# Kernel tuning notes

Hardware: AMD Instinct MI355X
Metric: run time of the kernel (lower is better)

The kernel has to match this reference:

```python
import jax, jax.numpy as jnp
import numpy as np
import math

N_WIRES = 8
DIM = 2 ** N_WIRES  # 256

# Pauli-Z sign table: wire 0 is the most-significant axis of the statevector.
_idx = np.arange(DIM)
_SIGNS = np.stack([1.0 - 2.0 * ((_idx >> (N_WIRES - 1 - w)) & 1) for w in range(N_WIRES)], axis=1).astype(np.float32)  # [256, 8]


def _cnot(state, c, t):
    # state: [N, 2, 2, ..., 2]; flip target axis where control bit == 1
    s0, s1 = jnp.split(state, 2, axis=1 + c)
    s1 = jnp.flip(s1, axis=1 + t)
    return jnp.concatenate([s0, s1], axis=1 + c)


def _quantum_heads(x, theta):
    """Simulate the QLayer circuit. x: [N, 8] -> PauliZ expectations [N, 8].

    Circuit: RX(x_i) then RX(theta_i) on wire i (commute -> RX(x_i+theta_i)),
    CNOT chain (0,1)...(6,7),(7,0), MeasureAll(PauliZ).
    """
    phi = 0.5 * (x + theta)  # RX half-angle
    c = jnp.cos(phi)
    s = jnp.sin(phi)
    # RX(a)|0> = cos(a/2)|0> - i sin(a/2)|1>
    amps = jax.lax.complex(jnp.stack([c, jnp.zeros_like(c)], axis=-1),
                           jnp.stack([jnp.zeros_like(s), -s], axis=-1))  # [N, 8, 2] complex64
    # Product state as rank-8 tensor [N, 2, ..., 2]
    state = amps[:, 0]
    for w in range(1, N_WIRES):
        state = state[..., None] * amps[:, w].reshape((-1,) + (1,) * w + (2,))
    # Entangling CNOT ring
    for w in range(N_WIRES - 1):
        state = _cnot(state, w, w + 1)
    state = _cnot(state, N_WIRES - 1, 0)
    probs = jnp.abs(state.reshape(-1, DIM)) ** 2  # [N, 256]
    return probs @ jnp.asarray(_SIGNS)  # [N, 8]


def setup_inputs() -> dict:
    key = jax.random.key(0)
    k1, k2, k3, k4 = jax.random.split(key, 4)
    B, S, E = 32, 512, 64
    return {
        "x": jax.random.normal(k1, (B, S, E), dtype=jnp.float32),
        "theta": jax.random.normal(k2, (N_WIRES,), dtype=jnp.float32),
        "W": jax.random.normal(k3, (E, E), dtype=jnp.float32) * 0.05,
        "b": jax.random.normal(k4, (E,), dtype=jnp.float32) * 0.05,
    }


def reference(x, theta, W, b):
    B, S, E = x.shape
    H = E // N_WIRES  # num_heads
    # q = k = v: same deterministic quantum projection applied to the same x.
    z = _quantum_heads(x.reshape(B * S * H, N_WIRES), theta).reshape(B, S, H, N_WIRES)
    scale = 1.0 / math.sqrt(E // H)
    # NOTE: matmul over last dims -> attention across heads within each token.
    scores = jnp.einsum('bshd,bstd->bsht', z, z) * scale  # [B, S, H, H]
    attn = jax.nn.softmax(scores, axis=-1)
    out = jnp.einsum('bsht,bstd->bshd', attn, z).reshape(B, S, E)
    return out @ W.T + b
```

## Files before the change

kernel.cpp:

```cpp
#include <hip/hip_runtime.h>


#define TOK_PER_BLK 16

typedef __attribute__((ext_vector_type(8))) short short8;
typedef __attribute__((ext_vector_type(4))) float f32x4;

__device__ inline unsigned short f2bf(float f) {
    unsigned u = __float_as_uint(f);
    u += 0x7FFF + ((u >> 16) & 1);
    return (unsigned short)(u >> 16);
}

__device__ inline short8 pack_bf16x8(float4 a, float4 b) {
    short8 r;
    r[0] = (short)f2bf(a.x); r[1] = (short)f2bf(a.y);
    r[2] = (short)f2bf(a.z); r[3] = (short)f2bf(a.w);
    r[4] = (short)f2bf(b.x); r[5] = (short)f2bf(b.y);
    r[6] = (short)f2bf(b.z); r[7] = (short)f2bf(b.w);
    return r;
}

__global__ __launch_bounds__(128, 2)
void mhaq_fused4(const float* __restrict__ x,
                 const float* __restrict__ theta,
                 const float* __restrict__ W,
                 const float* __restrict__ bias,
                 float* __restrict__ out,
                 int n_tokens)
{
    __shared__ __align__(16) float          zs[TOK_PER_BLK * 68];
    __shared__ __align__(16) unsigned short os[TOK_PER_BLK * 72];

    const int tid  = threadIdx.x;
    const int lane = tid & 63;
    const int wave = tid >> 6;
    const int lr   = lane & 15;
    const int lg   = lane >> 4;
    const int blockbase = blockIdx.x * TOK_PER_BLK;

    float4 wf[2][2][2];
    float  bj[2];
    {
        const float4* __restrict__ Wv = reinterpret_cast<const float4*>(W);
        #pragma unroll
        for (int nt = 0; nt < 2; ++nt) {
            int j = wave * 32 + nt * 16 + lr;
            bj[nt] = bias[j];
            #pragma unroll
            for (int kt = 0; kt < 2; ++kt) {
                int fidx = (j * 64 + kt * 32 + lg * 8) >> 2;
                wf[nt][kt][0] = Wv[fidx];
                wf[nt][kt][1] = Wv[fidx + 1];
            }
        }
    }

    const int tl = tid >> 3;
    const int g  = tid & 7;
    const int token = blockbase + tl;
    const bool valid = token < n_tokens;
    float zh[8];
    {
        float4 a  = make_float4(0.f, 0.f, 0.f, 0.f);
        float4 b4 = make_float4(0.f, 0.f, 0.f, 0.f);
        if (valid) {
            const float4* __restrict__ xp =
                reinterpret_cast<const float4*>(x) + (size_t)token * 16 + g * 2;
            a = xp[0]; b4 = xp[1];
        }
        float c0 = __cosf(a.x  + theta[0]);
        float c1 = __cosf(a.y  + theta[1]);
        float c2 = __cosf(a.z  + theta[2]);
        float c3 = __cosf(a.w  + theta[3]);
        float c4 = __cosf(b4.x + theta[4]);
        float c5 = __cosf(b4.y + theta[5]);
        float c6 = __cosf(b4.z + theta[6]);
        float c7 = __cosf(b4.w + theta[7]);
        float p1 = c0 * c1;
        float p2 = p1 * c2;
        float p3 = p2 * c3;
        float p4 = p3 * c4;
        float p5 = p4 * c5;
        float p6 = p5 * c6;
        float p7 = p6 * c7;
        float s6 = c6 * c7;
        float s5 = c5 * s6;
        float s4 = c4 * s5;
        float s3 = c3 * s4;
        float s2 = c2 * s3;
        float s1 = c1 * s2;
        zh[0] = s1; zh[1] = p1; zh[2] = p2; zh[3] = p3;
        zh[4] = p4; zh[5] = p5; zh[6] = p6; zh[7] = p7;

        float4* z4 = reinterpret_cast<float4*>(zs + tl * 68 + g * 8);
        z4[0] = make_float4(zh[0], zh[1], zh[2], zh[3]);
        z4[1] = make_float4(zh[4], zh[5], zh[6], zh[7]);
    }
    __syncthreads();

    {
        __align__(16) float zf[64];
        const float* zrow = zs + tl * 68;
        #pragma unroll
        for (int k4 = 0; k4 < 16; ++k4)
            *reinterpret_cast<float4*>(&zf[4 * k4]) =
                *reinterpret_cast<const float4*>(&zrow[4 * k4]);

        const float scale = 0.35355339059327373f;
        float sc[8];
        #pragma unroll
        for (int t = 0; t < 8; ++t) {
            float s = 0.f;
            #pragma unroll
            for (int d = 0; d < 8; ++d)
                s = fmaf(zh[d], zf[t * 8 + d], s);
            sc[t] = __expf(s * scale);
        }
        float sum = sc[0] + sc[1] + sc[2] + sc[3]
                  + sc[4] + sc[5] + sc[6] + sc[7];
        float inv = 1.0f / sum;

        unsigned short oh[8];
        #pragma unroll
        for (int d = 0; d < 8; ++d) {
            float acc = 0.f;
            #pragma unroll
            for (int t = 0; t < 8; ++t)
                acc = fmaf(sc[t], zf[t * 8 + d], acc);
            oh[d] = f2bf(acc * inv);
        }
        ushort4* o4 = reinterpret_cast<ushort4*>(&os[tl * 72 + g * 8]);
        o4[0] = make_ushort4(oh[0], oh[1], oh[2], oh[3]);
        o4[1] = make_ushort4(oh[4], oh[5], oh[6], oh[7]);
    }
    __syncthreads();

    {
        short8 afrag[2];
        #pragma unroll
        for (int kt = 0; kt < 2; ++kt)
            afrag[kt] = *reinterpret_cast<const short8*>(
                &os[lr * 72 + kt * 32 + lg * 8]);

        #pragma unroll
        for (int nt = 0; nt < 2; ++nt) {
            int j = wave * 32 + nt * 16 + lr;
            f32x4 acc = {bj[nt], bj[nt], bj[nt], bj[nt]};
            #pragma unroll
            for (int kt = 0; kt < 2; ++kt) {
                short8 bfrag = pack_bf16x8(wf[nt][kt][0], wf[nt][kt][1]);
                acc = __builtin_amdgcn_mfma_f32_16x16x32_bf16(
                    afrag[kt], bfrag, acc, 0, 0, 0);
            }
            #pragma unroll
            for (int r = 0; r < 4; ++r) {
                int trow = blockbase + lg * 4 + r;
                if (trow < n_tokens)
                    out[(size_t)trow * 64 + j] = acc[r];
            }
        }
    }
}

extern "C" void kernel_launch(void* const* d_in, const int* in_sizes, int n_in,
                              void* d_out, int out_size, void* d_ws, size_t ws_size,
                              hipStream_t stream)
{
    const float* x     = (const float*)d_in[0];
    const float* theta = (const float*)d_in[1];
    const float* W     = (const float*)d_in[2];
    const float* b     = (const float*)d_in[3];
    float* out         = (float*)d_out;

    const int n_tokens = in_sizes[0] / 64;
    const int blocks   = (n_tokens + TOK_PER_BLK - 1) / TOK_PER_BLK;
    mhaq_fused4<<<blocks, 128, 0, stream>>>(x, theta, W, b, out, n_tokens);
}
```

Baseline: 9.858 us.

## Double threads per block, split attention per head across two lanes

```diff
diff --git a/kernel.cpp b/kernel.cpp
--- a/kernel.cpp
+++ b/kernel.cpp
@@ -21,8 +21,8 @@
     return r;
 }
 
-__global__ __launch_bounds__(128, 2)
-void mhaq_fused4(const float* __restrict__ x,
+__global__ __launch_bounds__(256, 4)
+void mhaq_fused5(const float* __restrict__ x,
                  const float* __restrict__ theta,
                  const float* __restrict__ W,
                  const float* __restrict__ bias,
@@ -33,50 +33,48 @@
     __shared__ __align__(16) unsigned short os[TOK_PER_BLK * 72];
 
     const int tid  = threadIdx.x;
+    const int tl   = tid >> 4;
+    const int s    = tid & 15;
+    const int h    = s >> 1;
+    const int half = s & 1;
+    const int blockbase = blockIdx.x * TOK_PER_BLK;
+    const int token = blockbase + tl;
+    const bool zrole = (s < 8);
+
+    float4 xa = make_float4(0.f, 0.f, 0.f, 0.f);
+    float4 xb = make_float4(0.f, 0.f, 0.f, 0.f);
+    if (zrole && token < n_tokens) {
+        const float4* __restrict__ xp =
+            reinterpret_cast<const float4*>(x) + (size_t)token * 16 + s * 2;
+        xa = xp[0]; xb = xp[1];
+    }
+
     const int lane = tid & 63;
     const int wave = tid >> 6;
     const int lr   = lane & 15;
     const int lg   = lane >> 4;
-    const int blockbase = blockIdx.x * TOK_PER_BLK;
-
-    float4 wf[2][2][2];
-    float  bj[2];
+    const int j    = wave * 16 + lr;
+    float4 wf[2][2];
+    float  bj = bias[j];
     {
         const float4* __restrict__ Wv = reinterpret_cast<const float4*>(W);
         #pragma unroll
-        for (int nt = 0; nt < 2; ++nt) {
-            int j = wave * 32 + nt * 16 + lr;
-            bj[nt] = bias[j];
-            #pragma unroll
-            for (int kt = 0; kt < 2; ++kt) {
-                int fidx = (j * 64 + kt * 32 + lg * 8) >> 2;
-                wf[nt][kt][0] = Wv[fidx];
-                wf[nt][kt][1] = Wv[fidx + 1];
-            }
+        for (int kt = 0; kt < 2; ++kt) {
+            int fidx = (j * 64 + kt * 32 + lg * 8) >> 2;
+            wf[kt][0] = Wv[fidx];
+            wf[kt][1] = Wv[fidx + 1];
         }
     }
 
-    const int tl = tid >> 3;
-    const int g  = tid & 7;
-    const int token = blockbase + tl;
-    const bool valid = token < n_tokens;
-    float zh[8];
-    {
-        float4 a  = make_float4(0.f, 0.f, 0.f, 0.f);
-        float4 b4 = make_float4(0.f, 0.f, 0.f, 0.f);
-        if (valid) {
-            const float4* __restrict__ xp =
-                reinterpret_cast<const float4*>(x) + (size_t)token * 16 + g * 2;
-            a = xp[0]; b4 = xp[1];
-        }
-        float c0 = __cosf(a.x  + theta[0]);
-        float c1 = __cosf(a.y  + theta[1]);
-        float c2 = __cosf(a.z  + theta[2]);
-        float c3 = __cosf(a.w  + theta[3]);
-        float c4 = __cosf(b4.x + theta[4]);
-        float c5 = __cosf(b4.y + theta[5]);
-        float c6 = __cosf(b4.z + theta[6]);
-        float c7 = __cosf(b4.w + theta[7]);
+    if (zrole) {
+        float c0 = __cosf(xa.x + theta[0]);
+        float c1 = __cosf(xa.y + theta[1]);
+        float c2 = __cosf(xa.z + theta[2]);
+        float c3 = __cosf(xa.w + theta[3]);
+        float c4 = __cosf(xb.x + theta[4]);
+        float c5 = __cosf(xb.y + theta[5]);
+        float c6 = __cosf(xb.z + theta[6]);
+        float c7 = __cosf(xb.w + theta[7]);
         float p1 = c0 * c1;
         float p2 = p1 * c2;
         float p3 = p2 * c3;
@@ -90,49 +88,70 @@
         float s3 = c3 * s4;
         float s2 = c2 * s3;
         float s1 = c1 * s2;
-        zh[0] = s1; zh[1] = p1; zh[2] = p2; zh[3] = p3;
-        zh[4] = p4; zh[5] = p5; zh[6] = p6; zh[7] = p7;
-
-        float4* z4 = reinterpret_cast<float4*>(zs + tl * 68 + g * 8);
-        z4[0] = make_float4(zh[0], zh[1], zh[2], zh[3]);
-        z4[1] = make_float4(zh[4], zh[5], zh[6], zh[7]);
+        float4* z4 = reinterpret_cast<float4*>(zs + tl * 68 + s * 8);
+        z4[0] = make_float4(s1, p1, p2, p3);
+        z4[1] = make_float4(p4, p5, p6, p7);
     }
     __syncthreads();
 
     {
-        __align__(16) float zf[64];
         const float* zrow = zs + tl * 68;
+        float zh[8];
+        *reinterpret_cast<float4*>(&zh[0]) =
+            *reinterpret_cast<const float4*>(&zrow[h * 8]);
+        *reinterpret_cast<float4*>(&zh[4]) =
+            *reinterpret_cast<const float4*>(&zrow[h * 8 + 4]);
+
+        float zt[32];
         #pragma unroll
-        for (int k4 = 0; k4 < 16; ++k4)
-            *reinterpret_cast<float4*>(&zf[4 * k4]) =
-                *reinterpret_cast<const float4*>(&zrow[4 * k4]);
+        for (int i = 0; i < 8; ++i)
+            *reinterpret_cast<float4*>(&zt[i * 4]) =
+                *reinterpret_cast<const float4*>(&zrow[half * 32 + i * 4]);
 
         const float scale = 0.35355339059327373f;
-        float sc[8];
+        float e[4];
+        float psum = 0.f;
         #pragma unroll
-        for (int t = 0; t < 8; ++t) {
-            float s = 0.f;
+        for (int tt = 0; tt < 4; ++tt) {
+            float sd = 0.f;
             #pragma unroll
             for (int d = 0; d < 8; ++d)
-                s = fmaf(zh[d], zf[t * 8 + d], s);
-            sc[t] = __expf(s * scale);
+                sd = fmaf(zh[d], zt[tt * 8 + d], sd);
+            e[tt] = __expf(sd * scale);
+            psum += e[tt];
         }
-        float sum = sc[0] + sc[1] + sc[2] + sc[3]
-                  + sc[4] + sc[5] + sc[6] + sc[7];
-        float inv = 1.0f / sum;
+        float tot = psum + __shfl_xor(psum, 1, 64);
+        float inv = 1.0f / tot;
 
-        unsigned short oh[8];
+        float ep[4];
         #pragma unroll
-        for (int d = 0; d < 8; ++d) {
+        for (int tt = 0; tt < 4; ++tt)
+            ep[tt] = __shfl_xor(e[tt], 1, 64);
+
+        float ef[8];
+        #pragma unroll
+        for (int tt = 0; tt < 4; ++tt) {
+            ef[tt]     = half ? ep[tt] : e[tt];
+            ef[4 + tt] = half ? e[tt]  : ep[tt];
+        }
+
+        float zc[32];
+        #pragma unroll
+        for (int t = 0; t < 8; ++t)
+            *reinterpret_cast<float4*>(&zc[t * 4]) =
+                *reinterpret_cast<const float4*>(&zrow[t * 8 + half * 4]);
+
+        unsigned short oh[4];
+        #pragma unroll
+        for (int dd = 0; dd < 4; ++dd) {
             float acc = 0.f;
             #pragma unroll
             for (int t = 0; t < 8; ++t)
-                acc = fmaf(sc[t], zf[t * 8 + d], acc);
-            oh[d] = f2bf(acc * inv);
+                acc = fmaf(ef[t], zc[t * 4 + dd], acc);
+            oh[dd] = f2bf(acc * inv);
         }
-        ushort4* o4 = reinterpret_cast<ushort4*>(&os[tl * 72 + g * 8]);
-        o4[0] = make_ushort4(oh[0], oh[1], oh[2], oh[3]);
-        o4[1] = make_ushort4(oh[4], oh[5], oh[6], oh[7]);
+        *reinterpret_cast<ushort4*>(&os[tl * 72 + h * 8 + half * 4]) =
+            make_ushort4(oh[0], oh[1], oh[2], oh[3]);
     }
     __syncthreads();
 
@@ -143,22 +162,18 @@
             afrag[kt] = *reinterpret_cast<const short8*>(
                 &os[lr * 72 + kt * 32 + lg * 8]);
 
+        f32x4 acc = {bj, bj, bj, bj};
         #pragma unroll
-        for (int nt = 0; nt < 2; ++nt) {
-            int j = wave * 32 + nt * 16 + lr;
-            f32x4 acc = {bj[nt], bj[nt], bj[nt], bj[nt]};
-            #pragma unroll
-            for (int kt = 0; kt < 2; ++kt) {
-                short8 bfrag = pack_bf16x8(wf[nt][kt][0], wf[nt][kt][1]);
-                acc = __builtin_amdgcn_mfma_f32_16x16x32_bf16(
-                    afrag[kt], bfrag, acc, 0, 0, 0);
-            }
-            #pragma unroll
-            for (int r = 0; r < 4; ++r) {
-                int trow = blockbase + lg * 4 + r;
-                if (trow < n_tokens)
-                    out[(size_t)trow * 64 + j] = acc[r];
-            }
+        for (int kt = 0; kt < 2; ++kt) {
+            short8 bfrag = pack_bf16x8(wf[kt][0], wf[kt][1]);
+            acc = __builtin_amdgcn_mfma_f32_16x16x32_bf16(
+                afrag[kt], bfrag, acc, 0, 0, 0);
+        }
+        #pragma unroll
+        for (int r = 0; r < 4; ++r) {
+            int trow = blockbase + lg * 4 + r;
+            if (trow < n_tokens)
+                out[(size_t)trow * 64 + j] = acc[r];
         }
     }
 }
@@ -175,5 +190,5 @@
 
     const int n_tokens = in_sizes[0] / 64;
     const int blocks   = (n_tokens + TOK_PER_BLK - 1) / TOK_PER_BLK;
-    mhaq_fused4<<<blocks, 128, 0, stream>>>(x, theta, W, b, out, n_tokens);
+    mhaq_fused5<<<blocks, 256, 0, stream>>>(x, theta, W, b, out, n_tokens);
 }
```

Result: no change. 9.764 us (-1.0%).
